# Kernel optimization log

Measured on AMD Instinct MI355X. Metric: run time of the kernel, lower is better.

## Reference

```python
import jax, jax.numpy as jnp
import numpy as np
from jax import lax


def conv3x3(x, w):
    # torch Conv2d(k=3, s=1, p=1, bias=False) == cross-correlation, SAME padding
    return lax.conv_general_dilated(x, w, (1, 1), 'SAME',
                                    dimension_numbers=('NCHW', 'OIHW', 'NCHW'))


def pixel_shuffle4(x):
    # (N, C*16, H, W) -> (N, C, 4H, 4W), torch PixelShuffle semantics
    N, C16, H, W = x.shape
    r = 4
    C = C16 // (r * r)
    x = x.reshape(N, C, r, r, H, W)
    x = x.transpose(0, 1, 4, 2, 5, 3)  # N, C, H, r, W, r
    return x.reshape(N, C, H * r, W * r)


def pixel_conv(feat, kernel):
    # feat: (N, 1, H, W); kernel: (N, 25, H, W)
    # torch reference flattens patches with index = c*k*k + kw*k + kh
    # (due to permute(0,2,3,1,5,4)), so kernel channel j -> (kw=j//5, kh=j%5)
    N, C, H, W = feat.shape
    k, pad = 5, 2
    fp = jnp.pad(feat, ((0, 0), (0, 0), (pad, pad), (pad, pad)))
    ker = kernel.reshape(N, k, k, H, W)  # dims: (N, kw, kh, H, W)
    out = jnp.zeros_like(feat)
    for kw in range(k):
        for kh in range(k):
            out = out + fp[:, :, kh:kh + H, kw:kw + W] * ker[:, kw, kh][:, None]
    return out


def setup_inputs() -> dict:
    key = jax.random.key(0)
    ks = jax.random.split(key, 10)

    def w(k, o, i):
        fan_in = i * 9
        return jax.random.normal(k, (o, i, 3, 3), jnp.float32) * np.sqrt(2.0 / fan_in)

    return {
        'x': jax.random.normal(ks[0], (2, 1, 256, 256), jnp.float32),
        'w_e1': w(ks[1], 16, 1),
        'w_e2': w(ks[2], 32, 16),
        'w_e3': w(ks[3], 64, 32),
        'w_d1': w(ks[4], 32, 64),
        'w_d2': w(ks[5], 16, 32),
        'w_k1': w(ks[6], 32, 1),
        'w_k2': w(ks[7], 64, 32),
        'w_k3': w(ks[8], 32, 64),
        'w_k4': w(ks[9], 25, 32),
    }


def reference(x, w_e1, w_e2, w_e3, w_d1, w_d2, w_k1, w_k2, w_k3, w_k4):
    relu = jax.nn.relu
    # encoder
    h = relu(conv3x3(x, w_e1))
    h = relu(conv3x3(h, w_e2))
    h = relu(conv3x3(h, w_e3))
    # decoder
    h = relu(conv3x3(h, w_d1))
    h = relu(conv3x3(h, w_d2))
    # pixel shuffle + relu -> (N, 1, 4H, 4W)
    h = relu(pixel_shuffle4(h))
    # per-pixel kernel prediction branch
    z = relu(conv3x3(h, w_k1))
    z = relu(conv3x3(z, w_k2))
    z = relu(conv3x3(z, w_k3))
    z = relu(conv3x3(z, w_k4))  # (N, 25, 4H, 4W)
    z = pixel_conv(h, z)
    return h + z
```

## Files before the change

### kernel.cpp

```cpp
#include <hip/hip_runtime.h>


typedef float v2f __attribute__((ext_vector_type(2)));

template<int CIN, int COUT, int CB, int P, int W>
__global__ __launch_bounds__(256, 2) void conv3x3_relu_pk(
    const float* __restrict__ in, const float* __restrict__ wt,
    float* __restrict__ out,
    int in_y0, int in_rows, int out_y0, int out_rows)
{
  static_assert(COUT % CB == 0 && (CB & 1) == 0, "even CB dividing COUT");
  constexpr int NCB = COUT / CB;
  constexpr int TW  = 64;
  constexpr int TH  = 4 * P;
  constexpr int CBP = CB / 2;

  const int n   = blockIdx.z / NCB;
  const int co0 = (blockIdx.z % NCB) * CB;
  const int lx  = threadIdx.x & 63;
  const int yg  = threadIdx.x >> 6;
  const int x0  = blockIdx.x * TW;
  const int x   = x0 + lx;
  const int oy0 = out_y0 + blockIdx.y * TH;
  const int yb  = yg * P;

  const int maxoff = in_rows * W * 4 - 4;

  int   voff[P + 2][3];
  float mrow[P + 2];
#pragma unroll
  for (int r = 0; r < P + 2; ++r) {
    int ry = oy0 + yb + r - 1 - in_y0;
    mrow[r] = (ry >= 0 && ry < in_rows) ? 1.f : 0.f;
    int ryc = ry < 0 ? 0 : (ry >= in_rows ? in_rows - 1 : ry);
    int vo  = (ryc * W + x) * 4;
    voff[r][1] = vo;
    voff[r][0] = (vo > 4 ? vo : 4) - 4;
    int vr = vo + 4;
    voff[r][2] = vr < maxoff ? vr : maxoff;
  }
  const float ml = (x == 0)     ? 0.f : 1.f;
  const float mr = (x == W - 1) ? 0.f : 1.f;

  const bool interior =
      (x0 > 0) && (x0 + TW < W) &&
      ((oy0 - 1 - in_y0) >= 0) && ((oy0 + TH - in_y0) < in_rows);

  v2f acc[CBP][P];
#pragma unroll
  for (int jj = 0; jj < CBP; ++jj)
#pragma unroll
    for (int p = 0; p < P; ++p) acc[jj][p] = (v2f){0.f, 0.f};

  const float* inN = in + (size_t)n * CIN * in_rows * W;
  const size_t chbytes = (size_t)in_rows * W * 4;

#pragma unroll 1
  for (int ci = 0; ci < CIN; ++ci) {
    const char* bp = (const char*)inN + (size_t)ci * chbytes;

    float va[P + 2][3];
#pragma unroll
    for (int r = 0; r < P + 2; ++r)
#pragma unroll
      for (int c = 0; c < 3; ++c)
        va[r][c] = *(const float*)(bp + voff[r][c]);

    if (!interior) {
#pragma unroll
      for (int r = 0; r < P + 2; ++r) {
#pragma unroll
        for (int c = 0; c < 3; ++c) {
          float m = mrow[r];
          if (c == 0) m *= ml;
          if (c == 2) m *= mr;
          va[r][c] *= m;
        }
      }
    }

    __builtin_amdgcn_s_setprio(1);
#pragma unroll
    for (int jj = 0; jj < CBP; ++jj) {
      const float* wp0 = wt + ((size_t)(co0 + 2 * jj) * CIN + ci) * 9;
      const float* wp1 = wp0 + (size_t)CIN * 9;
      v2f w2[9];
#pragma unroll
      for (int t = 0; t < 9; ++t) w2[t] = (v2f){wp0[t], wp1[t]};
#pragma unroll
      for (int t = 0; t < 9; ++t) {
        const int r = t / 3, c = t - r * 3;
#pragma unroll
        for (int p = 0; p < P; ++p) {
          v2f tap = (v2f){va[p + r][c], va[p + r][c]};
          acc[jj][p] = __builtin_elementwise_fma(tap, w2[t], acc[jj][p]);
        }
      }
    }
    __builtin_amdgcn_s_setprio(0);
  }

  float* outN = out + (size_t)n * COUT * out_rows * W;
#pragma unroll
  for (int p = 0; p < P; ++p) {
    const int orow = (oy0 + yb + p) - out_y0;
    if (orow < out_rows) {
#pragma unroll
      for (int jj = 0; jj < CBP; ++jj) {
        float v0 = acc[jj][p][0], v1 = acc[jj][p][1];
        v0 = v0 < 0.f ? 0.f : v0;
        v1 = v1 < 0.f ? 0.f : v1;
        outN[((size_t)(co0 + 2 * jj) * out_rows + orow) * W + x] = v0;
        outN[((size_t)(co0 + 2 * jj + 1) * out_rows + orow) * W + x] = v1;
      }
    }
  }
}

template<int CIN, int COUT, int CB, int P, int W>
__global__ __launch_bounds__(256, 2) void conv3x3_relu_k(
    const float* __restrict__ in, const float* __restrict__ wt,
    float* __restrict__ out,
    int in_y0, int in_rows, int out_y0, int out_rows)
{
  static_assert(COUT % CB == 0, "CB must divide COUT");
  constexpr int NCB = COUT / CB;
  constexpr int TW  = 64;
  constexpr int TH  = 4 * P;

  const int n   = blockIdx.z / NCB;
  const int co0 = (blockIdx.z % NCB) * CB;
  const int lx  = threadIdx.x & 63;
  const int yg  = threadIdx.x >> 6;
  const int x0  = blockIdx.x * TW;
  const int x   = x0 + lx;
  const int oy0 = out_y0 + blockIdx.y * TH;
  const int yb  = yg * P;

  const int maxoff = in_rows * W * 4 - 4;

  int   voff[P + 2][3];
  float mrow[P + 2];
#pragma unroll
  for (int r = 0; r < P + 2; ++r) {
    int ry = oy0 + yb + r - 1 - in_y0;
    mrow[r] = (ry >= 0 && ry < in_rows) ? 1.f : 0.f;
    int ryc = ry < 0 ? 0 : (ry >= in_rows ? in_rows - 1 : ry);
    int vo  = (ryc * W + x) * 4;
    voff[r][1] = vo;
    voff[r][0] = (vo > 4 ? vo : 4) - 4;
    int vr = vo + 4;
    voff[r][2] = vr < maxoff ? vr : maxoff;
  }
  const float ml = (x == 0)     ? 0.f : 1.f;
  const float mr = (x == W - 1) ? 0.f : 1.f;

  const bool interior =
      (x0 > 0) && (x0 + TW < W) &&
      ((oy0 - 1 - in_y0) >= 0) && ((oy0 + TH - in_y0) < in_rows);

  float acc[CB][P];
#pragma unroll
  for (int j = 0; j < CB; ++j)
#pragma unroll
    for (int p = 0; p < P; ++p) acc[j][p] = 0.f;

  const float* inN = in + (size_t)n * CIN * in_rows * W;
  const size_t chbytes = (size_t)in_rows * W * 4;

#pragma unroll 1
  for (int ci = 0; ci < CIN; ++ci) {
    const char* bp = (const char*)inN + (size_t)ci * chbytes;

    float va[P + 2][3];
#pragma unroll
    for (int r = 0; r < P + 2; ++r)
#pragma unroll
      for (int c = 0; c < 3; ++c)
        va[r][c] = *(const float*)(bp + voff[r][c]);

    if (!interior) {
#pragma unroll
      for (int r = 0; r < P + 2; ++r) {
#pragma unroll
        for (int c = 0; c < 3; ++c) {
          float m = mrow[r];
          if (c == 0) m *= ml;
          if (c == 2) m *= mr;
          va[r][c] *= m;
        }
      }
    }

    __builtin_amdgcn_s_setprio(1);
#pragma unroll
    for (int j = 0; j < CB; ++j) {
      const float* wp = wt + ((size_t)(co0 + j) * CIN + ci) * 9;
      float w[9];
#pragma unroll
      for (int t = 0; t < 9; ++t) w[t] = wp[t];
#pragma unroll
      for (int t = 0; t < 9; ++t) {
        const int r = t / 3, c = t - r * 3;
#pragma unroll
        for (int p = 0; p < P; ++p)
          acc[j][p] = fmaf(va[p + r][c], w[t], acc[j][p]);
      }
    }
    __builtin_amdgcn_s_setprio(0);
  }

  float* outN = out + (size_t)n * COUT * out_rows * W;
#pragma unroll
  for (int p = 0; p < P; ++p) {
    const int orow = (oy0 + yb + p) - out_y0;
    if (orow < out_rows) {
#pragma unroll
      for (int j = 0; j < CB; ++j) {
        float v = acc[j][p] < 0.f ? 0.f : acc[j][p];
        outN[((size_t)(co0 + j) * out_rows + orow) * W + x] = v;
      }
    }
  }
}

__global__ __launch_bounds__(256) void pixel_shuffle_relu_k(
    const float* __restrict__ in, float* __restrict__ out)
{
  int i = blockIdx.x * 256 + threadIdx.x;
  int n = i >> 20;
  int p = i & 1048575;
  int x = p & 1023, y = p >> 10;
  int c = (y & 3) * 4 + (x & 3);
  float v = in[((size_t)(n * 16 + c) * 256 + (y >> 2)) * 256 + (x >> 2)];
  out[i] = v < 0.f ? 0.f : v;
}

__global__ __launch_bounds__(256) void pixel_conv_add_k(
    const float* __restrict__ h,
    const float* __restrict__ ker,
    float* __restrict__ out,
    int ky0, int krows)
{
  const int tx = threadIdx.x & 15, ty = threadIdx.x >> 4;
  const int x0 = blockIdx.x * 16;
  const int y0 = ky0 + blockIdx.y * 16;

  __shared__ float tile[20][21];
  for (int t = threadIdx.x; t < 20 * 20; t += 256) {
    int r = t / 20, c = t - r * 20;
    int yy = y0 + r - 2, xx = x0 + c - 2;
    float v = 0.f;
    if (yy >= 0 && yy < 1024 && xx >= 0 && xx < 1024) v = h[(size_t)yy * 1024 + xx];
    tile[r][c] = v;
  }
  __syncthreads();

  const int x = x0 + tx, y = y0 + ty;
  float acc = tile[ty + 2][tx + 2];
  const size_t kpix = (size_t)(y - ky0) * 1024 + x;
#pragma unroll
  for (int kw = 0; kw < 5; ++kw) {
#pragma unroll
    for (int kh = 0; kh < 5; ++kh) {
      float kv = ker[(size_t)(kw * 5 + kh) * krows * 1024 + kpix];
      acc = fmaf(tile[ty + kh][tx + kw], kv, acc);
    }
  }
  out[(size_t)y * 1024 + x] = acc;
}

extern "C" void kernel_launch(void* const* d_in, const int* in_sizes, int n_in,
                              void* d_out, int out_size, void* d_ws, size_t ws_size,
                              hipStream_t stream) {
  const float* x    = (const float*)d_in[0];
  const float* w_e1 = (const float*)d_in[1];
  const float* w_e2 = (const float*)d_in[2];
  const float* w_e3 = (const float*)d_in[3];
  const float* w_d1 = (const float*)d_in[4];
  const float* w_d2 = (const float*)d_in[5];
  const float* w_k1 = (const float*)d_in[6];
  const float* w_k2 = (const float*)d_in[7];
  const float* w_k3 = (const float*)d_in[8];
  const float* w_k4 = (const float*)d_in[9];

  const size_t HS_SZ = 8388608;
  const size_t AMIN  = 16777216;
  const size_t BMIN  = 33554432;

  int S = 64;
  {
    const int cand[5] = {1024, 512, 256, 128, 64};
    for (int i = 0; i < 5; ++i) {
      int s = cand[i];
      size_t a = 32ull * (size_t)(s + 6) * 1024 * 4; if (a < AMIN) a = AMIN;
      size_t b = 64ull * (size_t)(s + 4) * 1024 * 4; if (b < BMIN) b = BMIN;
      if (HS_SZ + a + b <= ws_size) { S = s; break; }
    }
  }
  size_t A_SZ = 32ull * (size_t)(S + 6) * 1024 * 4; if (A_SZ < AMIN) A_SZ = AMIN;

  char* ws = (char*)d_ws;
  float* Hs = (float*)(ws);
  float* A  = (float*)(ws + HS_SZ);
  float* B  = (float*)(ws + HS_SZ + A_SZ);
  float* outp = (float*)d_out;

  dim3 blk(256);

  conv3x3_relu_pk<1, 16, 16, 4, 256><<<dim3(4, 16, 2), blk, 0, stream>>>(x, w_e1, B, 0, 256, 0, 256);
  conv3x3_relu_pk<16, 32, 16, 4, 256><<<dim3(4, 16, 4), blk, 0, stream>>>(B, w_e2, A, 0, 256, 0, 256);
  conv3x3_relu_pk<32, 64, 16, 4, 256><<<dim3(4, 16, 8), blk, 0, stream>>>(A, w_e3, B, 0, 256, 0, 256);
  conv3x3_relu_pk<64, 32, 16, 4, 256><<<dim3(4, 16, 4), blk, 0, stream>>>(B, w_d1, A, 0, 256, 0, 256);
  conv3x3_relu_pk<32, 16, 16, 4, 256><<<dim3(4, 16, 2), blk, 0, stream>>>(A, w_d2, B, 0, 256, 0, 256);
  pixel_shuffle_relu_k<<<dim3(8192), blk, 0, stream>>>(B, Hs);

  const int nstr = 1024 / S;
  for (int n = 0; n < 2; ++n) {
    const float* himg = Hs + (size_t)n * 1048576;
    float* outn = outp + (size_t)n * 1048576;
    for (int s = 0; s < nstr; ++s) {
      const int r0 = s * S, r1 = r0 + S;
      const int z1y0 = (r0 - 3 > 0) ? r0 - 3 : 0;
      const int z1r  = ((r1 + 3 < 1024) ? r1 + 3 : 1024) - z1y0;
      const int z2y0 = (r0 - 2 > 0) ? r0 - 2 : 0;
      const int z2r  = ((r1 + 2 < 1024) ? r1 + 2 : 1024) - z2y0;
      const int z3y0 = (r0 - 1 > 0) ? r0 - 1 : 0;
      const int z3r  = ((r1 + 1 < 1024) ? r1 + 1 : 1024) - z3y0;
      const int g1 = (z1r + 15) / 16, g2 = (z2r + 15) / 16, g3 = (z3r + 15) / 16;

      conv3x3_relu_pk<1, 32, 16, 4, 1024><<<dim3(16, g1, 2), blk, 0, stream>>>(
          himg, w_k1, A, 0, 1024, z1y0, z1r);
      conv3x3_relu_pk<32, 64, 16, 4, 1024><<<dim3(16, g2, 4), blk, 0, stream>>>(
          A, w_k2, B, z1y0, z1r, z2y0, z2r);
      conv3x3_relu_pk<64, 32, 16, 4, 1024><<<dim3(16, g3, 2), blk, 0, stream>>>(
          B, w_k3, A, z2y0, z2r, z3y0, z3r);
      conv3x3_relu_k<32, 25, 25, 4, 1024><<<dim3(16, S / 16, 1), blk, 0, stream>>>(
          A, w_k4, B, z3y0, z3r, r0, S);
      pixel_conv_add_k<<<dim3(64, S / 16), blk, 0, stream>>>(
          himg, B, outn, r0, S);
    }
  }
}
```

Before: 2.682 ms.

## Batch both images through full-resolution kernel branch when workspace allows

```diff
diff --git a/kernel.cpp b/kernel.cpp
--- a/kernel.cpp
+++ b/kernel.cpp
@@ -242,6 +242,11 @@
     float* __restrict__ out,
     int ky0, int krows)
 {
+  const int nimg = blockIdx.z;
+  h   += (size_t)nimg * 1048576;
+  ker += (size_t)nimg * 25 * (size_t)krows * 1024;
+  out += (size_t)nimg * 1048576;
+
   const int tx = threadIdx.x & 15, ty = threadIdx.x >> 4;
   const int x0 = blockIdx.x * 16;
   const int y0 = ky0 + blockIdx.y * 16;
@@ -285,9 +290,41 @@
   const float* w_k4 = (const float*)d_in[9];
 
   const size_t HS_SZ = 8388608;
-  const size_t AMIN  = 16777216;
-  const size_t BMIN  = 33554432;
-
+  const size_t A2_SZ = 2ull * 32 * 1024 * 1024 * 4;
+  const size_t B2_SZ = 2ull * 64 * 1024 * 1024 * 4;
+  const bool batched = (HS_SZ + A2_SZ + B2_SZ <= ws_size);
+
+  char* ws = (char*)d_ws;
+  float* Hs   = (float*)(ws);
+  float* outp = (float*)d_out;
+  dim3 blk(256);
+
+  if (batched) {
+    float* A = (float*)(ws + HS_SZ);
+    float* B = (float*)(ws + HS_SZ + A2_SZ);
+
+    conv3x3_relu_pk<1, 16, 16, 4, 256><<<dim3(4, 16, 2), blk, 0, stream>>>(x, w_e1, B, 0, 256, 0, 256);
+    conv3x3_relu_pk<16, 32, 16, 4, 256><<<dim3(4, 16, 4), blk, 0, stream>>>(B, w_e2, A, 0, 256, 0, 256);
+    conv3x3_relu_pk<32, 64, 16, 4, 256><<<dim3(4, 16, 8), blk, 0, stream>>>(A, w_e3, B, 0, 256, 0, 256);
+    conv3x3_relu_pk<64, 32, 16, 4, 256><<<dim3(4, 16, 4), blk, 0, stream>>>(B, w_d1, A, 0, 256, 0, 256);
+    conv3x3_relu_pk<32, 16, 16, 4, 256><<<dim3(4, 16, 2), blk, 0, stream>>>(A, w_d2, B, 0, 256, 0, 256);
+    pixel_shuffle_relu_k<<<dim3(8192), blk, 0, stream>>>(B, Hs);
+
+    conv3x3_relu_pk<1, 32, 16, 4, 1024><<<dim3(16, 64, 4), blk, 0, stream>>>(
+        Hs, w_k1, A, 0, 1024, 0, 1024);
+    conv3x3_relu_pk<32, 64, 16, 4, 1024><<<dim3(16, 64, 8), blk, 0, stream>>>(
+        A, w_k2, B, 0, 1024, 0, 1024);
+    conv3x3_relu_pk<64, 32, 16, 4, 1024><<<dim3(16, 64, 4), blk, 0, stream>>>(
+        B, w_k3, A, 0, 1024, 0, 1024);
+    conv3x3_relu_k<32, 25, 25, 4, 1024><<<dim3(16, 64, 2), blk, 0, stream>>>(
+        A, w_k4, B, 0, 1024, 0, 1024);
+    pixel_conv_add_k<<<dim3(64, 64, 2), blk, 0, stream>>>(
+        Hs, B, outp, 0, 1024);
+    return;
+  }
+
+  const size_t AMIN = 16777216;
+  const size_t BMIN = 33554432;
   int S = 64;
   {
     const int cand[5] = {1024, 512, 256, 128, 64};
@@ -300,13 +337,8 @@
   }
   size_t A_SZ = 32ull * (size_t)(S + 6) * 1024 * 4; if (A_SZ < AMIN) A_SZ = AMIN;
 
-  char* ws = (char*)d_ws;
-  float* Hs = (float*)(ws);
-  float* A  = (float*)(ws + HS_SZ);
-  float* B  = (float*)(ws + HS_SZ + A_SZ);
-  float* outp = (float*)d_out;
-
-  dim3 blk(256);
+  float* A = (float*)(ws + HS_SZ);
+  float* B = (float*)(ws + HS_SZ + A_SZ);
 
   conv3x3_relu_pk<1, 16, 16, 4, 256><<<dim3(4, 16, 2), blk, 0, stream>>>(x, w_e1, B, 0, 256, 0, 256);
   conv3x3_relu_pk<16, 32, 16, 4, 256><<<dim3(4, 16, 4), blk, 0, stream>>>(B, w_e2, A, 0, 256, 0, 256);
@@ -337,7 +369,7 @@
           B, w_k3, A, z2y0, z2r, z3y0, z3r);
       conv3x3_relu_k<32, 25, 25, 4, 1024><<<dim3(16, S / 16, 1), blk, 0, stream>>>(
           A, w_k4, B, z3y0, z3r, r0, S);
-      pixel_conv_add_k<<<dim3(64, S / 16), blk, 0, stream>>>(
+      pixel_conv_add_k<<<dim3(64, S / 16, 1), blk, 0, stream>>>(
           himg, B, outn, r0, S);
     }
   }
```

Result: no change. 2.702 ms (+0.7%).
